# Kernel optimization log

Measured on AMD Instinct MI355X. Metric: run time of the kernel, lower is better.

Reference implementation:

```python
import jax, jax.numpy as jnp
import numpy as np

N_EMB = 4096
EMB_DIM = 256
BETA = 0.25


def setup_inputs() -> dict:
    key = jax.random.key(0)
    k1, k2 = jax.random.split(key)
    z = jax.random.normal(k1, (32, EMB_DIM, 32, 32), dtype=jnp.float32)
    # nn.Embedding weight initialized uniform(-1/n_emb, 1/n_emb)
    embedding = jax.random.uniform(
        k2, (N_EMB, EMB_DIM), dtype=jnp.float32,
        minval=-1.0 / N_EMB, maxval=1.0 / N_EMB)
    return {"z": z, "embedding": embedding}


def reference(z, embedding):
    sg = jax.lax.stop_gradient
    # (B,C,H,W) -> (B,H,W,C)
    zp = jnp.transpose(z, (0, 2, 3, 1))
    zf = zp.reshape(-1, EMB_DIM)  # [N, D]
    # squared distances: ||z||^2 + ||e||^2 - 2 z e^T  -> [N, n_emb]
    d = (jnp.sum(zf * zf, axis=1, keepdims=True)
         + jnp.sum(embedding * embedding, axis=1)
         - 2.0 * jnp.matmul(zf, embedding.T))
    idx = jnp.argmin(d, axis=1)  # [N]
    min_encodings = jax.nn.one_hot(idx, N_EMB, dtype=zf.dtype)  # [N, n_emb]
    e_mean = jnp.mean(min_encodings, axis=0)
    perplexity = jnp.exp(-jnp.sum(e_mean * jnp.log(e_mean + 1e-10)))
    # gather codebook rows (same math as one-hot matmul)
    z_q = jnp.take(embedding, idx, axis=0).reshape(zp.shape)
    # straight-through estimator
    z_q_st = zp + sg(z_q - zp)
    q_latent_loss = jnp.mean((z_q_st - sg(zp)) ** 2)
    e_latent_loss = jnp.mean((sg(z_q_st) - zp) ** 2)
    loss = q_latent_loss + BETA * e_latent_loss
    z_q_out = jnp.transpose(z_q_st, (0, 3, 1, 2))  # (B,C,H,W)
    return (loss, z_q_out, perplexity, min_encodings, idx[:, None])
```

## Files before the change

### kernel.cpp

```cpp
#include <hip/hip_runtime.h>

#define N_ROWS 32768
#define NEMB   4096
#define DIM    256

#define O_LOSS 0
#define O_ZQ   1ull
#define O_PERP 8388609ull
#define O_ENC  8388610ull
#define O_IDX  142606338ull
#define Z4_BEG 2097153
#define Z4_END 35651584

#define CAP    32
#define EPS    1e-3f

typedef unsigned long long u64;
typedef __attribute__((ext_vector_type(8))) __bf16 bf16x8;
typedef __attribute__((ext_vector_type(4))) float  f32x4;


__device__ __forceinline__ unsigned int f2bf1(float x) {
    unsigned int u = __float_as_uint(x);
    return (u + 0x7fffu + ((u >> 16) & 1u)) >> 16;
}
__device__ __forceinline__ unsigned int f2bf2(float lo, float hi) {
    return f2bf1(lo) | (f2bf1(hi) << 16);
}

__global__ __launch_bounds__(256)
void vq_prep(const float* __restrict__ z, const float* __restrict__ emb,
             unsigned short* __restrict__ zbf, unsigned short* __restrict__ embsw,
             int* __restrict__ counts, float* __restrict__ out)
{
    const int tid = threadIdx.x, blk = blockIdx.x;
    if (blk < 1024) {
        __shared__ float L[32][256];
        const int b = blk >> 5, sub = blk & 31;
        const int c0 = (sub >> 2) << 5;
        const int hw0 = (sub & 3) << 8;
        const float* zp = z + (size_t)b * 262144 + hw0 + tid;
#pragma unroll 8
        for (int i = 0; i < 32; ++i)
            L[i][tid] = zp[(size_t)(c0 + i) << 10];
        __syncthreads();
        const int n = (b << 10) + hw0 + tid;
        unsigned int pk[16];
#pragma unroll
        for (int c2 = 0; c2 < 16; ++c2)
            pk[c2] = f2bf2(L[2 * c2][tid], L[2 * c2 + 1][tid]);
        uint4* dst = (uint4*)((char*)zbf + (size_t)n * 512 + (size_t)c0 * 2);
#pragma unroll
        for (int q = 0; q < 4; ++q)
            dst[q] = make_uint4(pk[4*q], pk[4*q+1], pk[4*q+2], pk[4*q+3]);
    } else {
        const int base = ((blk - 1024) << 8) + tid;
#pragma unroll
        for (int q = 0; q < 4; ++q) {
            const int ch = (base << 2) + q;
            const int code = ch >> 5, cw = ch & 31;
            const float* ep = emb + (size_t)code * 256 + cw * 8;
            float4 e0 = *(const float4*)ep;
            float4 e1 = *(const float4*)(ep + 4);
            uint4 pk = make_uint4(f2bf2(e0.x, e0.y), f2bf2(e0.z, e0.w),
                                  f2bf2(e1.x, e1.y), f2bf2(e1.z, e1.w));
            *(uint4*)((char*)embsw + (size_t)code * 512 + (size_t)((cw ^ (code & 7)) << 4)) = pk;
        }
        if (blk == 1024) {
            for (int j = tid; j < NEMB; j += 256) counts[j] = 0;
            if (tid == 0) {
                out[O_ENC] = 0.f; out[O_ENC + 1] = 0.f;
                out[(size_t)Z4_END * 4] = 0.f; out[(size_t)Z4_END * 4 + 1] = 0.f;
            }
        }
    }
}

__global__ __launch_bounds__(512, 2)
void vq_filter(const float* __restrict__ z, const float* __restrict__ emb,
               const unsigned short* __restrict__ zbf_us,
               const unsigned short* __restrict__ embsw,
               float* __restrict__ out, u64* __restrict__ ws_best)
{
#pragma clang fp contract(off)
    __shared__ __align__(16) char Bsh[65536];
    __shared__ float zsumS[256];
    __shared__ float rowmaxS[256];
    __shared__ unsigned short rowlist[256][CAP];
    __shared__ int rowcnt[256];
    __shared__ int nflag;
    __shared__ int flagrows[32];
    __shared__ u64 flagbest[32];

    const int tid = threadIdx.x;
    const int blk = blockIdx.x;
    const int rb  = blk >> 1;
    const int hv  = blk & 1;
    const int n0  = rb << 8;
    const int C0  = hv << 11;
    const int b   = n0 >> 10;
    const int hw0 = n0 & 1023;
    const int w    = tid >> 6;
    const int lane = tid & 63;
    const int r0w  = w << 5;
    const int arow = lane & 15;
    const int akg  = lane >> 4;
    const float* zb = z + (size_t)b * 262144 + hw0;

    if (tid < 32) flagbest[tid] = ~0ull;
    if (tid == 0) nflag = 0;

    if (tid < 256) {
        rowcnt[tid] = 0;
        const float* gz = zb + tid;
        float hs0, hs1;
        {
            float r[8];
#pragma unroll
            for (int j = 0; j < 8; ++j) { float v = gz[(size_t)j << 10]; r[j] = v * v; }
            for (int m = 1; m < 16; ++m)
#pragma unroll
                for (int j = 0; j < 8; ++j) {
                    float v = gz[(size_t)(8 * m + j) << 10];
                    float sq = v * v;
                    r[j] = r[j] + sq;
                }
            hs0 = ((r[0] + r[1]) + (r[2] + r[3])) + ((r[4] + r[5]) + (r[6] + r[7]));
        }
        {
            float r[8];
#pragma unroll
            for (int j = 0; j < 8; ++j) { float v = gz[(size_t)(128 + j) << 10]; r[j] = v * v; }
            for (int m = 1; m < 16; ++m)
#pragma unroll
                for (int j = 0; j < 8; ++j) {
                    float v = gz[(size_t)(128 + 8 * m + j) << 10];
                    float sq = v * v;
                    r[j] = r[j] + sq;
                }
            hs1 = ((r[0] + r[1]) + (r[2] + r[3])) + ((r[4] + r[5]) + (r[6] + r[7]));
        }
        zsumS[tid] = hs0 + hs1;
    }

    bf16x8 A[2][8];
#pragma unroll
    for (int rf = 0; rf < 2; ++rf)
#pragma unroll
        for (int s = 0; s < 8; ++s)
            A[rf][s] = *(const bf16x8*)((const char*)zbf_us
                        + ((size_t)(n0 + r0w + rf * 16 + arow) << 9)
                        + (size_t)((s * 32 + akg * 8) << 1));

    auto stage = [&](int buf, int ct) {
        const char* sb = (const char*)embsw + (((size_t)(C0 + (ct << 6))) << 9)
                         + (w << 10) + (lane << 4);
        char* db = Bsh + buf * 32768 + (w << 10);
#pragma unroll
        for (int it = 0; it < 4; ++it) {
            __builtin_amdgcn_global_load_lds(
                (const __attribute__((address_space(1))) unsigned int*)(sb + it * 8192),
                (__attribute__((address_space(3))) unsigned int*)(db + it * 8192),
                16, 0, 0);
        }
    };

    float vmax[2][4];
#pragma unroll
    for (int rf = 0; rf < 2; ++rf)
#pragma unroll
        for (int j = 0; j < 4; ++j) vmax[rf][j] = -3.4e38f;
    float thr[2][4];

    const size_t zf_base = (size_t)Z4_BEG + (size_t)blk * 131072;

    for (int pass = 0; pass < 2; ++pass) {
        stage(0, 0);
        __syncthreads();
        for (int ct = 0; ct < 32; ++ct) {
            const int buf = ct & 1;
            if (ct < 31) stage(buf ^ 1, ct + 1);

            {
                const int iter = pass * 32 + ct;
                const size_t g = zf_base + (size_t)iter * 2048 + tid;
                const float4 zv = make_float4(0.f, 0.f, 0.f, 0.f);
#pragma unroll
                for (int q = 0; q < 4; ++q) {
                    const size_t i4 = g + (size_t)q * 512;
                    if (i4 < (size_t)Z4_END) ((float4*)out)[i4] = zv;
                }
            }

            f32x4 acc[2][4];
            const f32x4 zz = {0.f, 0.f, 0.f, 0.f};
#pragma unroll
            for (int rf = 0; rf < 2; ++rf)
#pragma unroll
                for (int cf = 0; cf < 4; ++cf) acc[rf][cf] = zz;

            const char* bufp = Bsh + buf * 32768;
#pragma unroll
            for (int s = 0; s < 8; ++s) {
#pragma unroll
                for (int cf = 0; cf < 4; ++cf) {
                    const int cl = (cf << 4) + arow;
                    const int off = (cl << 9) + (((s << 6) + (akg << 4)) ^ ((cl & 7) << 4));
                    bf16x8 bb = *(const bf16x8*)(bufp + off);
                    acc[0][cf] = __builtin_amdgcn_mfma_f32_16x16x32_bf16(A[0][s], bb, acc[0][cf], 0, 0, 0);
                    acc[1][cf] = __builtin_amdgcn_mfma_f32_16x16x32_bf16(A[1][s], bb, acc[1][cf], 0, 0, 0);
                }
            }

            if (pass == 0) {
#pragma unroll
                for (int rf = 0; rf < 2; ++rf)
#pragma unroll
                    for (int cf = 0; cf < 4; ++cf)
#pragma unroll
                        for (int j = 0; j < 4; ++j)
                            vmax[rf][j] = fmaxf(vmax[rf][j], acc[rf][cf][j]);
            } else {
#pragma unroll
                for (int rf = 0; rf < 2; ++rf)
#pragma unroll
                    for (int cf = 0; cf < 4; ++cf)
#pragma unroll
                        for (int j = 0; j < 4; ++j) {
                            const float v = acc[rf][cf][j];
                            if (v >= thr[rf][j]) {
                                const int row  = r0w + rf * 16 + akg * 4 + j;
                                const int code = (ct << 6) + (cf << 4) + arow;
                                const int slot = atomicAdd(&rowcnt[row], 1);
                                if (slot < CAP) rowlist[row][slot] = (unsigned short)code;
                                else if (slot == CAP) {
                                    const int fi = atomicAdd(&nflag, 1);
                                    if (fi < 32) flagrows[fi] = row;
                                }
                            }
                        }
            }
            __syncthreads();
        }
        if (pass == 0) {
#pragma unroll
            for (int rf = 0; rf < 2; ++rf)
#pragma unroll
                for (int j = 0; j < 4; ++j) {
                    float v = vmax[rf][j];
                    v = fmaxf(v, __shfl_xor(v, 1));
                    v = fmaxf(v, __shfl_xor(v, 2));
                    v = fmaxf(v, __shfl_xor(v, 4));
                    v = fmaxf(v, __shfl_xor(v, 8));
                    vmax[rf][j] = v;
                }
            if ((lane & 15) == 0) {
#pragma unroll
                for (int rf = 0; rf < 2; ++rf)
#pragma unroll
                    for (int j = 0; j < 4; ++j)
                        rowmaxS[r0w + rf * 16 + akg * 4 + j] = vmax[rf][j];
            }
            __syncthreads();
#pragma unroll
            for (int rf = 0; rf < 2; ++rf)
#pragma unroll
                for (int j = 0; j < 4; ++j)
                    thr[rf][j] = rowmaxS[r0w + rf * 16 + akg * 4 + j] - EPS;
        }
    }
    __syncthreads();

    if (tid < 256) {
        const int cnt = rowcnt[tid];
        if (cnt <= CAP) {
            const float zs = zsumS[tid];
            const float* zrow = zb + tid;
            u64 bestk = ~0ull;
            for (int basec = 0; basec < cnt; basec += 8) {
                int codes[8];
#pragma unroll
                for (int j = 0; j < 8; ++j) {
                    const int jj = basec + j;
                    codes[j] = rowlist[tid][jj < cnt ? jj : basec];
                }
                const float* ep[8];
#pragma unroll
                for (int j = 0; j < 8; ++j) ep[j] = emb + ((size_t)(C0 + codes[j]) << 8);
                float a8[8] = {0.f, 0.f, 0.f, 0.f, 0.f, 0.f, 0.f, 0.f};
#pragma unroll 2
                for (int k4 = 0; k4 < 64; ++k4) {
                    const float zv0 = zrow[(size_t)(4 * k4 + 0) << 10];
                    const float zv1 = zrow[(size_t)(4 * k4 + 1) << 10];
                    const float zv2 = zrow[(size_t)(4 * k4 + 2) << 10];
                    const float zv3 = zrow[(size_t)(4 * k4 + 3) << 10];
                    float4 e4[8];
#pragma unroll
                    for (int j = 0; j < 8; ++j) e4[j] = *(const float4*)(ep[j] + 4 * k4);
#pragma unroll
                    for (int j = 0; j < 8; ++j) {
                        a8[j] = fmaf(zv0, e4[j].x, a8[j]);
                        a8[j] = fmaf(zv1, e4[j].y, a8[j]);
                        a8[j] = fmaf(zv2, e4[j].z, a8[j]);
                        a8[j] = fmaf(zv3, e4[j].w, a8[j]);
                    }
                }
#pragma unroll
                for (int j = 0; j < 8; ++j) {
                    if (basec + j < cnt) {
                        const float d = fmaf(-2.f, a8[j], zs);
                        const u64 key = ((u64)__float_as_uint(d) << 32)
                                      | (unsigned)(C0 + codes[j]);
                        if (key < bestk) bestk = key;
                    }
                }
            }
            ws_best[((size_t)(n0 + tid) << 1) + hv] = bestk;
        }
    }
    __syncthreads();

    const int nf = (nflag > 32) ? 32 : nflag;
    for (int f = 0; f < nf; ++f) {
        const int fr = flagrows[f];
        if (tid < 256) {
            const float zs = zsumS[fr];
            const float* zrow = zb + fr;
            const float* ep0 = emb + ((size_t)(C0 + (tid << 3)) << 8);
            float a8[8] = {0.f, 0.f, 0.f, 0.f, 0.f, 0.f, 0.f, 0.f};
#pragma unroll 2
            for (int k4 = 0; k4 < 64; ++k4) {
                const float zv0 = zrow[(size_t)(4 * k4 + 0) << 10];
                const float zv1 = zrow[(size_t)(4 * k4 + 1) << 10];
                const float zv2 = zrow[(size_t)(4 * k4 + 2) << 10];
                const float zv3 = zrow[(size_t)(4 * k4 + 3) << 10];
#pragma unroll
                for (int j = 0; j < 8; ++j) {
                    const float4 e4 = *(const float4*)(ep0 + (size_t)j * 256 + 4 * k4);
                    a8[j] = fmaf(zv0, e4.x, a8[j]);
                    a8[j] = fmaf(zv1, e4.y, a8[j]);
                    a8[j] = fmaf(zv2, e4.z, a8[j]);
                    a8[j] = fmaf(zv3, e4.w, a8[j]);
                }
            }
            u64 bk = ~0ull;
#pragma unroll
            for (int j = 0; j < 8; ++j) {
                const float d = fmaf(-2.f, a8[j], zs);
                const u64 key = ((u64)__float_as_uint(d) << 32)
                              | (unsigned)(C0 + (tid << 3) + j);
                if (key < bk) bk = key;
            }
            atomicMin(&flagbest[f], bk);
        }
    }
    __syncthreads();
    if (tid < nf) ws_best[((size_t)(n0 + flagrows[tid]) << 1) + hv] = flagbest[tid];
}

__global__ void vq_scatter(const u64* __restrict__ ws_best, float* __restrict__ out,
                           int* __restrict__ counts, int* __restrict__ ws_idx)
{
    int i = blockIdx.x * 256 + threadIdx.x;
    if (i < N_ROWS) {
        u64 m = ws_best[(size_t)i * 2];
        u64 v = ws_best[(size_t)i * 2 + 1];
        if (v < m) m = v;
        int id = (int)(m & 0xffffffffu);
        ws_idx[i] = id;
        out[O_IDX + i] = (float)id;
        out[O_ENC + (size_t)i * 4096 + id] = 1.0f;
        atomicAdd(&counts[id], 1);
    }
}

__global__ __launch_bounds__(256)
void vq_zq(const float* __restrict__ z, const float* __restrict__ emb,
           const int* __restrict__ ws_idx, float* __restrict__ out,
           double* __restrict__ parts)
{
#pragma clang fp contract(off)
    double val = 0.0;
#pragma unroll 1
    for (int j = 0; j < 16; ++j) {
        const size_t gid = (size_t)blockIdx.x * 4096 + j * 256 + threadIdx.x;
        const int b   = (int)(gid >> 18);
        const int rem = (int)(gid & 262143);
        const int c   = rem >> 10;
        const int hw  = rem & 1023;
        const int n   = (b << 10) + hw;

        const float zp = z[gid];
        const float e  = emb[(size_t)ws_idx[n] * 256 + c];
        const float t  = e - zp;
        const float zq = zp + t;
        out[O_ZQ + gid] = zq;

        const float diff = zq - zp;
        val += (double)(diff * diff);
    }

    __shared__ double red[256];
    red[threadIdx.x] = val;
    __syncthreads();
    for (int st = 128; st > 0; st >>= 1) {
        if ((int)threadIdx.x < st) red[threadIdx.x] += red[threadIdx.x + st];
        __syncthreads();
    }
    if (threadIdx.x == 0) parts[blockIdx.x] = red[0];
}

__global__ void vq_final(const int* __restrict__ counts,
                         const double* __restrict__ parts, float* __restrict__ out)
{
    __shared__ double red[256];
    const int t = threadIdx.x;

    double loc = 0.0;
    for (int j = t; j < NEMB; j += 256) {
        float em = (float)counts[j] * (1.0f / 32768.0f);
        float lt = em + 1e-10f;
        float lg = logf(lt);
        float pr = em * lg;
        loc += (double)pr;
    }
    red[t] = loc;
    __syncthreads();
    for (int st = 128; st > 0; st >>= 1) {
        if (t < st) red[t] += red[t + st];
        __syncthreads();
    }
    double s = red[0];
    __syncthreads();

    double q = 0.0;
    for (int j = t; j < 2048; j += 256) q += parts[j];
    red[t] = q;
    __syncthreads();
    for (int st = 128; st > 0; st >>= 1) {
        if (t < st) red[t] += red[t + st];
        __syncthreads();
    }
    if (t == 0) {
        out[O_PERP] = expf(-(float)s);
        double qm = red[0] * (1.0 / 8388608.0);
        float  qf = (float)qm;
        out[O_LOSS] = qf + 0.25f * qf;
    }
}

extern "C" void kernel_launch(void* const* d_in, const int* in_sizes, int n_in,
                              void* d_out, int out_size, void* d_ws, size_t ws_size,
                              hipStream_t stream)
{
    const float* z   = (const float*)d_in[0];
    const float* emb = (const float*)d_in[1];
    float* out = (float*)d_out;

    u64*    ws_best = (u64*)d_ws;
    int*    counts  = (int*)((char*)d_ws + 1048576);
    double* parts   = (double*)((char*)d_ws + 1064960);
    int*    ws_idx  = (int*)((char*)d_ws + 1081344);

    unsigned short* zbf   = (unsigned short*)((char*)d_out + 16);
    unsigned short* embsw = (unsigned short*)((char*)d_out + 16 + 16777216);

    vq_prep   <<<1152, 256, 0, stream>>>(z, emb, zbf, embsw, counts, out);
    vq_filter <<<256,  512, 0, stream>>>(z, emb, zbf, embsw, out, ws_best);
    vq_scatter<<<128,  256, 0, stream>>>(ws_best, out, counts, ws_idx);
    vq_zq     <<<2048, 256, 0, stream>>>(z, emb, ws_idx, out, parts);
    vq_final  <<<1,    256, 0, stream>>>(counts, parts, out);
}
```

Measured before the change: 999.3 us.

## Stage gathered codebook rows in shared memory for z_q transpose write

The z_q kernel now assigns each block 32 spatial positions, loads their 32 selected codebook rows into a padded shared-memory tile with coalesced float4 reads, then writes the NCHW output from that tile. This replaces strided per-element global gathers from the embedding table with reused LDS reads. Output stores become nontemporal, and the grid is halved, so the final reduction reads 1024 partial sums. The zq kernel is a small part of the whole pipeline, so the effect on total time may be limited.

```diff
diff --git a/kernel.cpp b/kernel.cpp
--- a/kernel.cpp
+++ b/kernel.cpp
@@ -380,34 +380,58 @@
            double* __restrict__ parts)
 {
 #pragma clang fp contract(off)
+    __shared__ float embT[32][257];
+    __shared__ int idxS[32];
+    __shared__ double red[256];
+
+    const int tid = threadIdx.x;
+    const int blk = blockIdx.x;
+    const int b   = blk >> 5;
+    const int hw0 = (blk & 31) << 5;
+    const int n0  = (b << 10) + hw0;
+
+    if (tid < 32) idxS[tid] = ws_idx[n0 + tid];
+    __syncthreads();
+
+    {
+        const int g = tid >> 3, l8 = tid & 7;
+        const float* er = emb + (size_t)idxS[g] * 256;
+#pragma unroll
+        for (int it = 0; it < 8; ++it) {
+            const float4 v = *(const float4*)(er + it * 32 + l8 * 4);
+            const int c = it * 32 + l8 * 4;
+            embT[g][c]     = v.x;
+            embT[g][c + 1] = v.y;
+            embT[g][c + 2] = v.z;
+            embT[g][c + 3] = v.w;
+        }
+    }
+    __syncthreads();
+
+    const int r  = tid & 31;
+    const int cq = tid >> 5;
+    const size_t base = (size_t)b * 262144 + hw0 + r;
     double val = 0.0;
-#pragma unroll 1
-    for (int j = 0; j < 16; ++j) {
-        const size_t gid = (size_t)blockIdx.x * 4096 + j * 256 + threadIdx.x;
-        const int b   = (int)(gid >> 18);
-        const int rem = (int)(gid & 262143);
-        const int c   = rem >> 10;
-        const int hw  = rem & 1023;
-        const int n   = (b << 10) + hw;
-
+#pragma unroll 4
+    for (int i = 0; i < 32; ++i) {
+        const int c = i * 8 + cq;
+        const size_t gid = base + (size_t)c * 1024;
         const float zp = z[gid];
-        const float e  = emb[(size_t)ws_idx[n] * 256 + c];
+        const float e  = embT[r][c];
         const float t  = e - zp;
         const float zq = zp + t;
-        out[O_ZQ + gid] = zq;
-
+        __builtin_nontemporal_store(zq, &out[O_ZQ + gid]);
         const float diff = zq - zp;
         val += (double)(diff * diff);
     }
 
-    __shared__ double red[256];
-    red[threadIdx.x] = val;
+    red[tid] = val;
     __syncthreads();
     for (int st = 128; st > 0; st >>= 1) {
-        if ((int)threadIdx.x < st) red[threadIdx.x] += red[threadIdx.x + st];
+        if (tid < st) red[tid] += red[tid + st];
         __syncthreads();
     }
-    if (threadIdx.x == 0) parts[blockIdx.x] = red[0];
+    if (tid == 0) parts[blk] = red[0];
 }
 
 __global__ void vq_final(const int* __restrict__ counts,
@@ -434,7 +458,7 @@
     __syncthreads();
 
     double q = 0.0;
-    for (int j = t; j < 2048; j += 256) q += parts[j];
+    for (int j = t; j < 1024; j += 256) q += parts[j];
     red[t] = q;
     __syncthreads();
     for (int st = 128; st > 0; st >>= 1) {
@@ -468,6 +492,6 @@
     vq_prep   <<<1152, 256, 0, stream>>>(z, emb, zbf, embsw, counts, out);
     vq_filter <<<256,  512, 0, stream>>>(z, emb, zbf, embsw, out, ws_best);
     vq_scatter<<<128,  256, 0, stream>>>(ws_best, out, counts, ws_idx);
-    vq_zq     <<<2048, 256, 0, stream>>>(z, emb, ws_idx, out, parts);
+    vq_zq     <<<1024, 256, 0, stream>>>(z, emb, ws_idx, out, parts);
     vq_final  <<<1,    256, 0, stream>>>(counts, parts, out);
 }
```

Measured after the change: 953.1 us. -4.6%, faster.
